# Optimization experiments

Measured on AMD Instinct MI355X. Metric: run time of the kernel, lower is better.

The kernel has to match this reference:

```python
import jax, jax.numpy as jnp
import numpy as np

N_NODES = 50000
N_EDGES = 600000
D_FEAT = 128


def setup_inputs() -> dict:
    key = jax.random.key(0)
    k_h, k_src, k_dst, k_dt, k_norm = jax.random.split(key, 5)
    h = jax.random.normal(k_h, (N_NODES, D_FEAT), dtype=jnp.float32)
    src = jax.random.randint(k_src, (N_EDGES,), 0, N_NODES, dtype=jnp.int32)
    dst = jax.random.randint(k_dst, (N_EDGES,), 0, N_NODES, dtype=jnp.int32)
    # dt: non-negative time deltas (scaled up a bit so the decay matters)
    dt = jax.random.uniform(k_dt, (N_EDGES,), dtype=jnp.float32) * 10.0
    # norm: symmetric-normalization-like positive edge weights
    norm = jax.random.uniform(k_norm, (N_EDGES,), dtype=jnp.float32)
    decay_lam = jnp.full((1,), 0.1, dtype=jnp.float32)  # nn.Parameter(0.1)
    return {"h": h, "src": src, "dst": dst, "dt": dt, "norm": norm, "decay_lam": decay_lam}


def reference(h, src, dst, dt, norm, decay_lam):
    # lam = relu(decay_lam) + 1e-4  (scalar)
    lam = jax.nn.relu(decay_lam[0]) + 1e-4
    # per-edge temporal weight: norm * exp(-lam * dt)   [E]
    w = norm * jnp.exp(-lam * dt)
    # u_mul_e: gather source features, scale by edge weight  [E, D]
    m = h[src] * w[:, None]
    # sum-reduce messages at destination nodes  [N, D]
    h_new = jax.ops.segment_sum(m, dst, num_segments=h.shape[0])
    return h_new
```

## Files before the change

### kernel.cpp

```cpp
#include <hip/hip_runtime.h>
#include <hip/hip_bf16.h>

#define D_FEAT 128
#define BIN_SHIFT 7
#define NODES_PER_BIN 128
#define BCAP 4096
#define EPB 2048
#define T1 512
#define CSR_L_CAP 6016
#define OVF_CAP 4096

typedef float f2v __attribute__((ext_vector_type(2)));

__device__ __forceinline__ unsigned bf16_rne(float f) {
    unsigned u = __float_as_uint(f);
    return (u + 0x7fffu + ((u >> 16) & 1u)) >> 16;
}

__global__ void __launch_bounds__(T1)
conv_bin_kernel(const float* __restrict__ h,
                const int* __restrict__ src, const int* __restrict__ dst,
                const float* __restrict__ dt, const float* __restrict__ norm,
                const float* __restrict__ decay_lam,
                unsigned* __restrict__ hb,
                int* __restrict__ bin_cursor, unsigned long long* __restrict__ binned,
                int* __restrict__ ovf_cnt, int* __restrict__ ovf_d,
                int* __restrict__ ovf_s, float* __restrict__ ovf_w,
                int E, int HN4, int convBlocks, int NB) {
    __shared__ unsigned hist[T1];
    __shared__ unsigned cur[T1];
    __shared__ unsigned gbase[T1];

    int t = threadIdx.x;
    if (blockIdx.x < convBlocks) {
        int i = blockIdx.x * T1 + t;
        if (i < HN4) {
            float4 v = ((const float4*)h)[i];
            ((uint2*)hb)[i] = make_uint2(bf16_rne(v.x) | (bf16_rne(v.y) << 16),
                                         bf16_rne(v.z) | (bf16_rne(v.w) << 16));
        }
        return;
    }

    int e0 = (blockIdx.x - convBlocks) * EPB;

    hist[t] = 0; cur[t] = 0;
    __syncthreads();

    float lam = fmaxf(decay_lam[0], 0.0f) + 1e-4f;

    unsigned long long ent[EPB / T1];
    int bn[EPB / T1];
    #pragma unroll
    for (int k = 0; k < EPB / T1; ++k) {
        int e = e0 + k * T1 + t;
        bn[k] = -1;
        if (e < E) {
            int s = src[e], d = dst[e];
            float w = norm[e] * expf(-lam * dt[e]);
            int b = d >> BIN_SHIFT;
            int l = d & (NODES_PER_BIN - 1);
            ent[k] = ((unsigned long long)l << 32) | (((unsigned)s << 16) | bf16_rne(w));
            bn[k] = b;
            atomicAdd(&hist[b], 1u);
        }
    }
    __syncthreads();

    if (t < NB && hist[t] > 0)
        gbase[t] = (unsigned)atomicAdd(&bin_cursor[t], (int)hist[t]);
    __syncthreads();

    #pragma unroll
    for (int k = 0; k < EPB / T1; ++k) {
        if (bn[k] >= 0) {
            int b = bn[k];
            unsigned gp = gbase[b] + atomicAdd(&cur[b], 1u);
            if (gp < BCAP) {
                binned[(size_t)b * BCAP + gp] = ent[k];
            } else {
                int o = atomicAdd(ovf_cnt, 1);
                if (o < OVF_CAP) {
                    int l = (int)(ent[k] >> 32);
                    ovf_d[o] = (b << BIN_SHIFT) | l;
                    ovf_s[o] = (int)((ent[k] >> 16) & 0xFFFFu);
                    ovf_w[o] = __uint_as_float(((unsigned)ent[k] & 0xFFFFu) << 16);
                }
            }
        }
    }
}

__global__ void __launch_bounds__(T1, 2)
sort_gather_kernel(const unsigned long long* __restrict__ binned,
                   const int* __restrict__ bin_cursor,
                   const unsigned* __restrict__ hb,
                   const int* __restrict__ ovf_cnt, const int* __restrict__ ovf_d,
                   const int* __restrict__ ovf_s, const float* __restrict__ ovf_w,
                   float* __restrict__ out, int N) {
    __shared__ unsigned hist[NODES_PER_BIN];
    __shared__ unsigned padoff[NODES_PER_BIN];
    __shared__ unsigned cur[NODES_PER_BIN];
    __shared__ unsigned csr_l[CSR_L_CAP];
    __shared__ unsigned wtot;

    int b = blockIdx.x;
    int t = threadIdx.x;
    int cnt = min(bin_cursor[b], BCAP);

    if (t < NODES_PER_BIN) { hist[t] = 0; cur[t] = 0; }
    for (int i = t; i < CSR_L_CAP; i += T1) csr_l[i] = 0;
    __syncthreads();

    unsigned long long ent[BCAP / T1];
    size_t base_in = (size_t)b * BCAP;
    #pragma unroll
    for (int k = 0; k < BCAP / T1; ++k) {
        int idx = k * T1 + t;
        ent[k] = ~0ull;
        if (idx < cnt) {
            unsigned long long e = binned[base_in + idx];
            ent[k] = e;
            atomicAdd(&hist[(int)(e >> 32)], 1u);
        }
    }
    __syncthreads();

    unsigned pc = 0, val = 0;
    if (t < NODES_PER_BIN) { pc = (hist[t] + 15u) & ~15u; val = pc; }
    #pragma unroll
    for (int off = 1; off < 64; off <<= 1) {
        unsigned u = __shfl_up(val, off, 64);
        if ((t & 63) >= off) val += u;
    }
    if (t == 63) wtot = val;
    __syncthreads();
    if (t < NODES_PER_BIN)
        padoff[t] = val + ((t >= 64) ? wtot : 0u) - pc;
    __syncthreads();

    #pragma unroll
    for (int k = 0; k < BCAP / T1; ++k) {
        if (ent[k] != ~0ull) {
            int l = (int)(ent[k] >> 32);
            unsigned p = padoff[l] + atomicAdd(&cur[l], 1u);
            csr_l[p] = (unsigned)ent[k];
        }
    }
    __syncthreads();

    int wid = t >> 6;
    int lane = t & 63;
    int nodes = min(NODES_PER_BIN, N - (b << BIN_SHIFT));
    bool ovf_bin = bin_cursor[b] > BCAP;

    for (int l = wid; l < nodes; l += 8) {
        unsigned base = padoff[l];
        unsigned mr = (hist[l] + 15u) & ~15u;
        float accx = 0.0f, accy = 0.0f;
        for (unsigned j = 0; j < mr; j += 16) {
            unsigned uu[16];
            unsigned vv[16];
            #pragma unroll
            for (int q = 0; q < 16; ++q) uu[q] = csr_l[base + j + q];
            #pragma unroll
            for (int q = 0; q < 16; ++q)
                vv[q] = hb[(size_t)(uu[q] >> 16) * 64 + lane];
            #pragma unroll
            for (int q = 0; q < 16; ++q) {
                float wf = __uint_as_float(uu[q] << 16);
                accx += __uint_as_float(vv[q] << 16) * wf;
                accy += __uint_as_float(vv[q] & 0xffff0000u) * wf;
            }
        }
        int node = (b << BIN_SHIFT) + l;
        if (ovf_bin) {
            int oc = min(*ovf_cnt, OVF_CAP);
            for (int o = 0; o < oc; ++o) {
                if (ovf_d[o] == node) {
                    float we = ovf_w[o];
                    unsigned v = hb[(size_t)ovf_s[o] * 64 + lane];
                    accx += __uint_as_float(v << 16) * we;
                    accy += __uint_as_float(v & 0xffff0000u) * we;
                }
            }
        }
        f2v r;
        r.x = accx; r.y = accy;
        __builtin_nontemporal_store(r, (f2v*)(out + (size_t)node * D_FEAT) + lane);
    }
}


__global__ void degree_kernel(const int* __restrict__ dst, int* __restrict__ deg, int E) {
    int e = blockIdx.x * blockDim.x + threadIdx.x;
    if (e >= E) return;
    atomicAdd(&deg[dst[e]], 1);
}

__global__ void scan_blocks(const int* __restrict__ deg, int* __restrict__ offs,
                            int* __restrict__ blockSums, int N) {
    __shared__ int tmp[256];
    int tid = threadIdx.x;
    int gid = blockIdx.x * 256 + tid;
    int v = (gid < N) ? deg[gid] : 0;
    tmp[tid] = v;
    __syncthreads();
    for (int off = 1; off < 256; off <<= 1) {
        int t = (tid >= off) ? tmp[tid - off] : 0;
        __syncthreads();
        tmp[tid] += t;
        __syncthreads();
    }
    if (gid < N) offs[gid] = tmp[tid] - v;
    if (tid == 255) blockSums[blockIdx.x] = tmp[255];
}

__global__ void scan_sums(int* __restrict__ blockSums, int* __restrict__ blockOffs, int nb) {
    __shared__ int tmp[256];
    int tid = threadIdx.x;
    int v = (tid < nb) ? blockSums[tid] : 0;
    tmp[tid] = v;
    __syncthreads();
    for (int off = 1; off < 256; off <<= 1) {
        int t = (tid >= off) ? tmp[tid - off] : 0;
        __syncthreads();
        tmp[tid] += t;
        __syncthreads();
    }
    if (tid < nb) blockOffs[tid] = tmp[tid] - v;
}

__global__ void scan_fixup(int* __restrict__ offs, const int* __restrict__ blockOffs,
                           int* __restrict__ cursor, int N) {
    int gid = blockIdx.x * 256 + threadIdx.x;
    if (gid >= N) return;
    int o = offs[gid] + blockOffs[blockIdx.x];
    offs[gid] = o;
    cursor[gid] = o;
}

__global__ void bucket_kernel(const int* __restrict__ src, const int* __restrict__ dst,
                              const float* __restrict__ dt, const float* __restrict__ norm,
                              const float* __restrict__ decay_lam,
                              int* __restrict__ cursor, float2* __restrict__ pairs, int E) {
    int e = blockIdx.x * blockDim.x + threadIdx.x;
    if (e >= E) return;
    float lam = fmaxf(decay_lam[0], 0.0f) + 1e-4f;
    float w = norm[e] * expf(-lam * dt[e]);
    int d = dst[e];
    int pos = atomicAdd(&cursor[d], 1);
    float2 p;
    p.x = __int_as_float(src[e]);
    p.y = w;
    pairs[pos] = p;
}

__global__ void __launch_bounds__(256)
gather_kernel(const float* __restrict__ h,
              const int* __restrict__ offs, const int* __restrict__ deg,
              const float2* __restrict__ pairs, float* __restrict__ out, int N) {
    int node = blockIdx.x * 4 + (threadIdx.x >> 6);
    if (node >= N) return;
    int lane = threadIdx.x & 63;
    int start = offs[node];
    int end = start + deg[node];
    float accx = 0.0f, accy = 0.0f;
    for (int j = start; j < end; ++j) {
        float2 p = pairs[j];
        int s = __float_as_int(p.x);
        float we = p.y;
        float2 v = ((const float2*)(h + (size_t)s * D_FEAT))[lane];
        accx += v.x * we;
        accy += v.y * we;
    }
    float2 r; r.x = accx; r.y = accy;
    ((float2*)(out + (size_t)node * D_FEAT))[lane] = r;
}

extern "C" void kernel_launch(void* const* d_in, const int* in_sizes, int n_in,
                              void* d_out, int out_size, void* d_ws, size_t ws_size,
                              hipStream_t stream) {
    const float* h         = (const float*)d_in[0];
    const int*   src       = (const int*)d_in[1];
    const int*   dst       = (const int*)d_in[2];
    const float* dt        = (const float*)d_in[3];
    const float* norm      = (const float*)d_in[4];
    const float* decay_lam = (const float*)d_in[5];
    float* out = (float*)d_out;

    const int E  = in_sizes[1];
    const int HN = in_sizes[0];
    const int N  = out_size / D_FEAT;
    const int NB = (N + NODES_PER_BIN - 1) >> BIN_SHIFT;

    auto align64 = [](size_t x) { return (x + 63) & ~(size_t)63; };
    size_t sz_binc = align64((size_t)NB * 4);
    size_t sz_ovfc = 64;
    size_t sz_ovf  = align64((size_t)OVF_CAP * 4);
    size_t sz_binn = align64((size_t)NB * BCAP * 8);
    size_t sz_hb   = align64((size_t)HN * 2);
    size_t need = sz_binc + sz_ovfc + 3 * sz_ovf + sz_binn + sz_hb;

    if (ws_size >= need && N <= 65536 && (HN & 3) == 0 && NB <= T1) {
        char* ws = (char*)d_ws;
        int* bin_cursor = (int*)ws;                 ws += sz_binc;
        int* ovf_cnt    = (int*)ws;                 ws += sz_ovfc;
        int* ovf_d      = (int*)ws;                 ws += sz_ovf;
        int* ovf_s      = (int*)ws;                 ws += sz_ovf;
        float* ovf_w    = (float*)ws;               ws += sz_ovf;
        unsigned long long* binned = (unsigned long long*)ws;  ws += sz_binn;
        unsigned* hb    = (unsigned*)ws;

        hipMemsetAsync(bin_cursor, 0, sz_binc + sz_ovfc, stream);

        const int HN4 = HN / 4;
        const int convBlocks = (HN4 + T1 - 1) / T1;
        const int binBlocks  = (E + EPB - 1) / EPB;
        conv_bin_kernel<<<convBlocks + binBlocks, T1, 0, stream>>>(
            h, src, dst, dt, norm, decay_lam, hb, bin_cursor, binned,
            ovf_cnt, ovf_d, ovf_s, ovf_w, E, HN4, convBlocks, NB);

        sort_gather_kernel<<<NB, T1, 0, stream>>>(
            binned, bin_cursor, hb, ovf_cnt, ovf_d, ovf_s, ovf_w, out, N);
    } else {
        const int nb = (N + 255) / 256;
        char* ws = (char*)d_ws;
        int*    dega      = (int*)ws;     ws += (size_t)N * 4;
        int*    offsa     = (int*)ws;     ws += (size_t)N * 4;
        int*    cursor    = (int*)ws;     ws += (size_t)N * 4;
        int*    blockSums = (int*)ws;     ws += 256 * 4;
        int*    blockOffs = (int*)ws;     ws += 256 * 4;
        float2* pairs     = (float2*)ws;

        hipMemsetAsync(dega, 0, (size_t)N * 4, stream);
        degree_kernel<<<(E + 255) / 256, 256, 0, stream>>>(dst, dega, E);
        scan_blocks<<<nb, 256, 0, stream>>>(dega, offsa, blockSums, N);
        scan_sums<<<1, 256, 0, stream>>>(blockSums, blockOffs, nb);
        scan_fixup<<<nb, 256, 0, stream>>>(offsa, blockOffs, cursor, N);
        bucket_kernel<<<(E + 255) / 256, 256, 0, stream>>>(
            src, dst, dt, norm, decay_lam, cursor, pairs, E);
        gather_kernel<<<(N + 3) / 4, 256, 0, stream>>>(h, offsa, dega, pairs, out, N);
    }
}
```

Measured before the change: 127.9 us.

## Use small 16-node bins with single-wave gather blocks and fixed binning grid

Shrinks destination bins from 128 to 16 nodes, which gives about 3125 bins instead of 391, and runs the sort/gather kernel with one 64-thread wave per bin instead of 512 threads. The binning kernel now uses a fixed 256 blocks, each holding up to 8 edges per thread, with shared histograms sized for up to 3200 bins. The aim is more, smaller gather blocks for better load balance and occupancy, and fewer large-block syncs. The cost is more global atomics on bin cursors, a larger shared histogram in the binning kernel, and each wave handling its 16 nodes one after another.

```diff
diff --git a/kernel.cpp b/kernel.cpp
--- a/kernel.cpp
+++ b/kernel.cpp
@@ -2,12 +2,14 @@
 #include <hip/hip_bf16.h>
 
 #define D_FEAT 128
-#define BIN_SHIFT 7
-#define NODES_PER_BIN 128
-#define BCAP 4096
-#define EPB 2048
+#define BIN_SHIFT 4
+#define NODES_PER_BIN 16
+#define BCAP 1024
+#define NB_MAX 3200
 #define T1 512
-#define CSR_L_CAP 6016
+#define BINB 256
+#define RMAX 8
+#define CSR_CAP 1280
 #define OVF_CAP 4096
 
 typedef float f2v __attribute__((ext_vector_type(2)));
@@ -27,9 +29,9 @@
                 int* __restrict__ ovf_cnt, int* __restrict__ ovf_d,
                 int* __restrict__ ovf_s, float* __restrict__ ovf_w,
                 int E, int HN4, int convBlocks, int NB) {
-    __shared__ unsigned hist[T1];
-    __shared__ unsigned cur[T1];
-    __shared__ unsigned gbase[T1];
+    __shared__ unsigned hist[NB_MAX];
+    __shared__ unsigned cur[NB_MAX];
+    __shared__ unsigned gbase[NB_MAX];
 
     int t = threadIdx.x;
     if (blockIdx.x < convBlocks) {
@@ -42,20 +44,24 @@
         return;
     }
 
-    int e0 = (blockIdx.x - convBlocks) * EPB;
-
-    hist[t] = 0; cur[t] = 0;
+    int blk = blockIdx.x - convBlocks;
+    int e_begin = (int)((long long)blk * E / BINB);
+    int e_end   = (int)((long long)(blk + 1) * E / BINB);
+    int cnt_e   = e_end - e_begin;
+
+    for (int i = t; i < NB; i += T1) { hist[i] = 0; cur[i] = 0; }
     __syncthreads();
 
     float lam = fmaxf(decay_lam[0], 0.0f) + 1e-4f;
 
-    unsigned long long ent[EPB / T1];
-    int bn[EPB / T1];
+    unsigned long long ent[RMAX];
+    int bn[RMAX];
     #pragma unroll
-    for (int k = 0; k < EPB / T1; ++k) {
-        int e = e0 + k * T1 + t;
+    for (int k = 0; k < RMAX; ++k) {
+        int i = k * T1 + t;
         bn[k] = -1;
-        if (e < E) {
+        if (i < cnt_e) {
+            int e = e_begin + i;
             int s = src[e], d = dst[e];
             float w = norm[e] * expf(-lam * dt[e]);
             int b = d >> BIN_SHIFT;
@@ -67,12 +73,13 @@
     }
     __syncthreads();
 
-    if (t < NB && hist[t] > 0)
-        gbase[t] = (unsigned)atomicAdd(&bin_cursor[t], (int)hist[t]);
+    for (int i = t; i < NB; i += T1)
+        if (hist[i] > 0)
+            gbase[i] = (unsigned)atomicAdd(&bin_cursor[i], (int)hist[i]);
     __syncthreads();
 
     #pragma unroll
-    for (int k = 0; k < EPB / T1; ++k) {
+    for (int k = 0; k < RMAX; ++k) {
         if (bn[k] >= 0) {
             int b = bn[k];
             unsigned gp = gbase[b] + atomicAdd(&cur[b], 1u);
@@ -91,7 +98,7 @@
     }
 }
 
-__global__ void __launch_bounds__(T1, 2)
+__global__ void __launch_bounds__(64)
 sort_gather_kernel(const unsigned long long* __restrict__ binned,
                    const int* __restrict__ bin_cursor,
                    const unsigned* __restrict__ hb,
@@ -101,60 +108,43 @@
     __shared__ unsigned hist[NODES_PER_BIN];
     __shared__ unsigned padoff[NODES_PER_BIN];
     __shared__ unsigned cur[NODES_PER_BIN];
-    __shared__ unsigned csr_l[CSR_L_CAP];
-    __shared__ unsigned wtot;
+    __shared__ unsigned csr_l[CSR_CAP];
 
     int b = blockIdx.x;
     int t = threadIdx.x;
     int cnt = min(bin_cursor[b], BCAP);
+    size_t rbase = (size_t)b * BCAP;
 
     if (t < NODES_PER_BIN) { hist[t] = 0; cur[t] = 0; }
-    for (int i = t; i < CSR_L_CAP; i += T1) csr_l[i] = 0;
-    __syncthreads();
-
-    unsigned long long ent[BCAP / T1];
-    size_t base_in = (size_t)b * BCAP;
-    #pragma unroll
-    for (int k = 0; k < BCAP / T1; ++k) {
-        int idx = k * T1 + t;
-        ent[k] = ~0ull;
-        if (idx < cnt) {
-            unsigned long long e = binned[base_in + idx];
-            ent[k] = e;
-            atomicAdd(&hist[(int)(e >> 32)], 1u);
-        }
-    }
+    for (int i = t; i < CSR_CAP; i += 64) csr_l[i] = 0;
+    __syncthreads();
+
+    for (int i = t; i < cnt; i += 64)
+        atomicAdd(&hist[(int)(binned[rbase + i] >> 32)], 1u);
     __syncthreads();
 
     unsigned pc = 0, val = 0;
     if (t < NODES_PER_BIN) { pc = (hist[t] + 15u) & ~15u; val = pc; }
     #pragma unroll
-    for (int off = 1; off < 64; off <<= 1) {
+    for (int off = 1; off < NODES_PER_BIN; off <<= 1) {
         unsigned u = __shfl_up(val, off, 64);
-        if ((t & 63) >= off) val += u;
-    }
-    if (t == 63) wtot = val;
-    __syncthreads();
-    if (t < NODES_PER_BIN)
-        padoff[t] = val + ((t >= 64) ? wtot : 0u) - pc;
-    __syncthreads();
-
-    #pragma unroll
-    for (int k = 0; k < BCAP / T1; ++k) {
-        if (ent[k] != ~0ull) {
-            int l = (int)(ent[k] >> 32);
-            unsigned p = padoff[l] + atomicAdd(&cur[l], 1u);
-            csr_l[p] = (unsigned)ent[k];
-        }
-    }
-    __syncthreads();
-
-    int wid = t >> 6;
-    int lane = t & 63;
+        if (t >= off) val += u;
+    }
+    if (t < NODES_PER_BIN) padoff[t] = val - pc;
+    __syncthreads();
+
+    for (int i = t; i < cnt; i += 64) {
+        unsigned long long e = binned[rbase + i];
+        int l = (int)(e >> 32);
+        unsigned p = padoff[l] + atomicAdd(&cur[l], 1u);
+        csr_l[p] = (unsigned)e;
+    }
+    __syncthreads();
+
     int nodes = min(NODES_PER_BIN, N - (b << BIN_SHIFT));
     bool ovf_bin = bin_cursor[b] > BCAP;
 
-    for (int l = wid; l < nodes; l += 8) {
+    for (int l = 0; l < nodes; ++l) {
         unsigned base = padoff[l];
         unsigned mr = (hist[l] + 15u) & ~15u;
         float accx = 0.0f, accy = 0.0f;
@@ -165,7 +155,7 @@
             for (int q = 0; q < 16; ++q) uu[q] = csr_l[base + j + q];
             #pragma unroll
             for (int q = 0; q < 16; ++q)
-                vv[q] = hb[(size_t)(uu[q] >> 16) * 64 + lane];
+                vv[q] = hb[(size_t)(uu[q] >> 16) * 64 + t];
             #pragma unroll
             for (int q = 0; q < 16; ++q) {
                 float wf = __uint_as_float(uu[q] << 16);
@@ -179,7 +169,7 @@
             for (int o = 0; o < oc; ++o) {
                 if (ovf_d[o] == node) {
                     float we = ovf_w[o];
-                    unsigned v = hb[(size_t)ovf_s[o] * 64 + lane];
+                    unsigned v = hb[(size_t)ovf_s[o] * 64 + t];
                     accx += __uint_as_float(v << 16) * we;
                     accy += __uint_as_float(v & 0xffff0000u) * we;
                 }
@@ -187,7 +177,7 @@
         }
         f2v r;
         r.x = accx; r.y = accy;
-        __builtin_nontemporal_store(r, (f2v*)(out + (size_t)node * D_FEAT) + lane);
+        __builtin_nontemporal_store(r, (f2v*)(out + (size_t)node * D_FEAT) + t);
     }
 }
 
@@ -302,7 +292,8 @@
     size_t sz_hb   = align64((size_t)HN * 2);
     size_t need = sz_binc + sz_ovfc + 3 * sz_ovf + sz_binn + sz_hb;
 
-    if (ws_size >= need && N <= 65536 && (HN & 3) == 0 && NB <= T1) {
+    if (ws_size >= need && N <= 65536 && (HN & 3) == 0 &&
+        NB <= NB_MAX && E <= BINB * T1 * RMAX) {
         char* ws = (char*)d_ws;
         int* bin_cursor = (int*)ws;                 ws += sz_binc;
         int* ovf_cnt    = (int*)ws;                 ws += sz_ovfc;
@@ -316,12 +307,11 @@
 
         const int HN4 = HN / 4;
         const int convBlocks = (HN4 + T1 - 1) / T1;
-        const int binBlocks  = (E + EPB - 1) / EPB;
-        conv_bin_kernel<<<convBlocks + binBlocks, T1, 0, stream>>>(
+        conv_bin_kernel<<<convBlocks + BINB, T1, 0, stream>>>(
             h, src, dst, dt, norm, decay_lam, hb, bin_cursor, binned,
             ovf_cnt, ovf_d, ovf_s, ovf_w, E, HN4, convBlocks, NB);
 
-        sort_gather_kernel<<<NB, T1, 0, stream>>>(
+        sort_gather_kernel<<<NB, 64, 0, stream>>>(
             binned, bin_cursor, hb, ovf_cnt, ovf_d, ovf_s, ovf_w, out, N);
     } else {
         const int nb = (N + 255) / 256;
```

Result: slower. 136.0 us (+6.3%).
